# Performance work log

Measured on AMD Instinct MI355X. Metric: run time of the kernel, lower is better.

## Reference

```python
import jax, jax.numpy as jnp
import numpy as np

BETA = 0.25


def setup_inputs() -> dict:
    key = jax.random.key(0)
    k1, k2 = jax.random.split(key)
    z_e = jax.random.normal(k1, (16, 64, 64, 64), dtype=jnp.float32)  # (B, D, H, W)
    embedding = jax.random.normal(k2, (1024, 64), dtype=jnp.float32)  # (K, D)
    return {"z_e": z_e, "embedding": embedding}


def reference(z_e, embedding):
    B, D, H, W = z_e.shape
    # (B, D, H, W) -> (B, H, W, D) -> (N, D)
    flat = jnp.transpose(z_e, (0, 2, 3, 1)).reshape(-1, D)
    # squared L2 distances to codebook: (N, K)
    dist = (jnp.sum(flat * flat, axis=1, keepdims=True)
            + jnp.sum(embedding * embedding, axis=1)
            - 2.0 * flat @ embedding.T)
    indices = jnp.argmin(dist, axis=1)  # (N,)
    z_q_flat = embedding[indices]  # (N, D) gather
    z_q = jnp.transpose(z_q_flat.reshape(B, H, W, D), (0, 3, 1, 2))  # (B, D, H, W)
    codebook_loss = jnp.mean((jax.lax.stop_gradient(z_q) - z_e) ** 2)
    commit_loss = jnp.mean((z_q - jax.lax.stop_gradient(z_e)) ** 2)
    vq_loss = codebook_loss + BETA * commit_loss
    # straight-through estimator
    z_q_st = z_e + jax.lax.stop_gradient(z_q - z_e)
    return (z_q_st, vq_loss, indices.reshape(B, H, W))
```

## Files before the change

### kernel.cpp

```cpp
#include <hip/hip_runtime.h>
#include <math.h>

typedef short  short8 __attribute__((ext_vector_type(8)));
typedef float  f32x4  __attribute__((ext_vector_type(4)));

#define ZQ_ELEMS 4194304
#define KC       1024
#define EPS_HALF 0.005f
#define PXB      128


__device__ inline unsigned short bf16_rne(float f) {
    union { float fv; unsigned u; } a; a.fv = f;
    unsigned r = a.u + 0x7FFFu + ((a.u >> 16) & 1u);
    return (unsigned short)(r >> 16);
}
__device__ inline float bf16_to_f(unsigned short h) {
    union { unsigned u; float fv; } a; a.u = ((unsigned)h) << 16;
    return a.fv;
}
__device__ inline double dpack(float hi, unsigned lo) {
    return __hiloint2double(__float_as_int(hi), (int)lo);
}
__device__ inline float dhi(double d) { return __int_as_float(__double2hiint(d)); }
__device__ inline unsigned dlo(double d) { return (unsigned)__double2loint(d); }

__global__ __launch_bounds__(256) void vq_prep(const float* __restrict__ emb,
        unsigned short* __restrict__ epack, float* __restrict__ enorm,
        float* __restrict__ out) {
    const int k = blockIdx.x * 256 + threadIdx.x;
    if (k == 0) out[ZQ_ELEMS] = 0.f;
    const float4* e4 = (const float4*)(emb + k * 64);
    float s = 0.f;
#pragma unroll
    for (int j = 0; j < 16; ++j) {
        float4 v = e4[j];
        float vv[4] = {v.x, v.y, v.z, v.w};
        ushort4 hv, lv;
        unsigned short h[4], l[4];
#pragma unroll
        for (int t = 0; t < 4; ++t) {
            s = fmaf(vv[t], vv[t], s);
            h[t] = bf16_rne(vv[t]);
            l[t] = bf16_rne(vv[t] - bf16_to_f(h[t]));
        }
        hv.x = h[0]; hv.y = h[1]; hv.z = h[2]; hv.w = h[3];
        lv.x = l[0]; lv.y = l[1]; lv.z = l[2]; lv.w = l[3];
        *(ushort4*)(epack + k * 128 + j * 4)      = hv;
        *(ushort4*)(epack + k * 128 + 64 + j * 4) = lv;
    }
    enorm[k] = s;
}

__global__ __launch_bounds__(256, 2) void vq_scan(const float* __restrict__ z_e,
        const unsigned short* __restrict__ epack, const float* __restrict__ enorm,
        double* __restrict__ pbest, float* __restrict__ pb2) {
    const int tid  = threadIdx.x;
    const int lane = tid & 63;
    const int col  = lane & 15;
    const int g    = lane >> 4;
    const int wv   = __builtin_amdgcn_readfirstlane(tid >> 6);
    const int pxblock = blockIdx.x >> 2;
    const int grp     = blockIdx.x & 3;
    const int cbase   = grp * 256 + wv * 64;
    const int pblk    = pxblock * PXB;

    __shared__ __align__(16) unsigned short afrag[PXB * 128];
    __shared__ double mrgB[4][PXB];
    __shared__ float  mrgS[4][PXB];

    {
        const int lp   = tid & 127;
        const int half = tid >> 7;
        const int pg   = pblk + lp;
        const float* zb = z_e + (pg >> 12) * 262144 + (pg & 4095);
        const int sx = (lp & 7) << 3;
#pragma unroll
        for (int s8 = 0; s8 < 4; ++s8) {
            const int d0 = half * 32 + s8 * 8;
            short8 H, L;
#pragma unroll
            for (int j = 0; j < 8; ++j) {
                float v = zb[(d0 + j) * 4096];
                unsigned short h = bf16_rne(v);
                H[j] = (short)h;
                L[j] = (short)bf16_rne(v - bf16_to_f(h));
            }
            const int sw = d0 ^ sx;
            *(short8*)&afrag[lp * 128 + sw]      = H;
            *(short8*)&afrag[lp * 128 + 64 + sw] = L;
        }
    }

    short8 ah[4][2], al[4][2];
    f32x4 enf[4];
    int clo[4][4];
    const int K1 = 1023 - cbase - g * 4;
#pragma unroll
    for (int t = 0; t < 4; ++t) {
        const int code = cbase + t * 16 + col;
        const short8* ph = (const short8*)(epack + code * 128) + g;
        ah[t][0] = ph[0]; ah[t][1] = ph[4];
        al[t][0] = ph[8]; al[t][1] = ph[12];
        const float4 e4 = *(const float4*)(enorm + cbase + t * 16 + g * 4);
        enf[t][0] = -0.5f * e4.x; enf[t][1] = -0.5f * e4.y;
        enf[t][2] = -0.5f * e4.z; enf[t][3] = -0.5f * e4.w;
#pragma unroll
        for (int r = 0; r < 4; ++r) clo[t][r] = K1 - t * 16 - r;
    }
    __syncthreads();

    const f32x4 zero4 = {0.f, 0.f, 0.f, 0.f};
    const int g8 = g * 8;

#pragma unroll 2
    for (int it = 0; it < PXB / 16; ++it) {
        const int lpx = it * 16 + col;
        const int sxp = (lpx & 7) << 3;
        const unsigned short* ap = &afrag[lpx * 128];
        const short8 bh0 = *(const short8*)&ap[(g8        ) ^ sxp];
        const short8 bh1 = *(const short8*)&ap[(32 + g8   ) ^ sxp];
        const short8 bl0 = *(const short8*)&ap[64 + ((g8     ) ^ sxp)];
        const short8 bl1 = *(const short8*)&ap[64 + ((32 + g8) ^ sxp)];

        double B = dpack(-INFINITY, 0u);
        float  S = -INFINITY;
#pragma unroll
        for (int t = 0; t < 4; ++t) {
            f32x4 aA, aB;
            aA = __builtin_amdgcn_mfma_f32_16x16x32_bf16(ah[t][0], bh0, enf[t], 0, 0, 0);
            aB = __builtin_amdgcn_mfma_f32_16x16x32_bf16(ah[t][1], bh1, zero4, 0, 0, 0);
            aA = __builtin_amdgcn_mfma_f32_16x16x32_bf16(al[t][0], bh0, aA, 0, 0, 0);
            aB = __builtin_amdgcn_mfma_f32_16x16x32_bf16(al[t][1], bh1, aB, 0, 0, 0);
            aA = __builtin_amdgcn_mfma_f32_16x16x32_bf16(ah[t][0], bl0, aA, 0, 0, 0);
            aB = __builtin_amdgcn_mfma_f32_16x16x32_bf16(ah[t][1], bl1, aB, 0, 0, 0);
#pragma unroll
            for (int r = 0; r < 4; ++r) {
                const float v = aA[r] + aB[r];
                S = __builtin_amdgcn_fmed3f(dhi(B), S, v);
                B = fmax(B, dpack(v, (unsigned)clo[t][r]));
            }
        }
#pragma unroll
        for (int s = 16; s < 64; s <<= 1) {
            const double ob = __shfl_xor(B, s, 64);
            const float  o2 = __shfl_xor(S, s, 64);
            S = __builtin_amdgcn_fmed3f(dhi(B), dhi(ob), fmaxf(S, o2));
            B = fmax(B, ob);
        }
        if (g == 0) { mrgB[wv][lpx] = B; mrgS[wv][lpx] = S; }
    }

    __syncthreads();
    if (tid < PXB) {
        double B = mrgB[0][tid];
        float  S = mrgS[0][tid];
#pragma unroll
        for (int w = 1; w < 4; ++w) {
            const double ob = mrgB[w][tid];
            const float  o2 = mrgS[w][tid];
            S = __builtin_amdgcn_fmed3f(dhi(B), dhi(ob), fmaxf(S, o2));
            B = fmax(B, ob);
        }
        const int pxg = pblk + tid;
        pbest[grp * 65536 + pxg] = B;
        pb2[grp * 65536 + pxg]   = S;
    }
}

__global__ __launch_bounds__(256) void vq_final(const float* __restrict__ z_e,
        const float* __restrict__ emb, const double* __restrict__ pbest,
        const float* __restrict__ pb2, float* __restrict__ out) {
    __shared__ float zq[64][65];
    __shared__ int   sidx[64];
    __shared__ unsigned long long smask;
    __shared__ float sred[4];
    const int tid  = threadIdx.x;
    const int lane = tid & 63;
    const int w    = __builtin_amdgcn_readfirstlane(tid >> 6);
    const int pblk = blockIdx.x * 64;
    const int batch = pblk >> 12;
    const int hw0   = pblk & 4095;

    if (w == 0) {
        const int px = pblk + lane;
        double B = pbest[px];
        float  S = pb2[px];
#pragma unroll
        for (int gq = 1; gq < 4; ++gq) {
            const double ob = pbest[gq * 65536 + px];
            const float  o2 = pb2[gq * 65536 + px];
            S = __builtin_amdgcn_fmed3f(dhi(B), dhi(ob), fmaxf(S, o2));
            B = fmax(B, ob);
        }
        sidx[lane] = 1023 - (int)dlo(B);
        const unsigned long long m = __ballot(dhi(B) - S < EPS_HALF);
        if (lane == 0) smask = m;
    }
    __syncthreads();

    {
        unsigned long long m = smask;
        int item = 0;
        while (m) {
            const int i = __builtin_ctzll(m);
            m &= m - 1;
            if ((item & 3) == w) {
                const int pix = pblk + i;
                const float* zb = z_e + (pix >> 12) * 262144 + (pix & 4095);
                float f[64];
#pragma unroll
                for (int d = 0; d < 64; ++d) f[d] = zb[d * 4096];
                double best = INFINITY; int bk = KC;
                for (int j = 0; j < 16; ++j) {
                    const int k = j * 64 + lane;
                    const float* e = emb + k * 64;
                    double a0 = 0.0, a1 = 0.0;
#pragma unroll
                    for (int d = 0; d < 64; d += 2) {
                        double d0 = (double)f[d]     - (double)e[d];
                        double d1 = (double)f[d + 1] - (double)e[d + 1];
                        a0 = fma(d0, d0, a0);
                        a1 = fma(d1, d1, a1);
                    }
                    double acc = a0 + a1;
                    if (acc < best || (acc == best && k < bk)) { best = acc; bk = k; }
                }
                for (int off = 32; off; off >>= 1) {
                    double ov = __shfl_down(best, off, 64);
                    int    oi = __shfl_down(bk, off, 64);
                    if (ov < best || (ov == best && oi < bk)) { best = ov; bk = oi; }
                }
                if (lane == 0) sidx[i] = bk;
            }
            ++item;
        }
    }
    __syncthreads();

    if (tid < 64) out[ZQ_ELEMS + 1 + pblk + tid] = (float)sidx[tid];

#pragma unroll
    for (int i = 0; i < 16; ++i) {
        const int p = w * 16 + i;
        const int k = sidx[p];
        zq[p][lane] = emb[k * 64 + lane];
    }
    __syncthreads();

    const int p4 = (tid & 15) * 4;
    const float* zeb = z_e + batch * 262144 + hw0;
    float* ob = out + batch * 262144 + hw0;
    float ss = 0.f;
#pragma unroll
    for (int it = 0; it < 4; ++it) {
        const int d = (tid >> 4) + it * 16;
        float4 q;
        q.x = zq[p4 + 0][d]; q.y = zq[p4 + 1][d];
        q.z = zq[p4 + 2][d]; q.w = zq[p4 + 3][d];
        const float4 z = *(const float4*)(zeb + d * 4096 + p4);
        *(float4*)(ob + d * 4096 + p4) = q;
        const float d0 = q.x - z.x, d1 = q.y - z.y, d2 = q.z - z.z, d3 = q.w - z.w;
        ss += d0 * d0 + d1 * d1 + d2 * d2 + d3 * d3;
    }
    for (int off = 32; off; off >>= 1) ss += __shfl_down(ss, off, 64);
    if (lane == 0) sred[w] = ss;
    __syncthreads();
    if (tid == 0)
        atomicAdd(out + ZQ_ELEMS,
                  ((sred[0] + sred[1]) + (sred[2] + sred[3])) * (1.25f / (float)ZQ_ELEMS));
}

extern "C" void kernel_launch(void* const* d_in, const int* in_sizes, int n_in,
                              void* d_out, int out_size, void* d_ws, size_t ws_size,
                              hipStream_t stream) {
    const float* z_e = (const float*)d_in[0];
    const float* emb = (const float*)d_in[1];
    float* out = (float*)d_out;
    char* ws = (char*)d_ws;
    unsigned short* epack = (unsigned short*)ws;
    float*  enorm = (float*)(ws + 262144);
    double* pbest = (double*)(ws + 524288);
    float*  pb2   = (float*)(ws + 2621440);

    vq_prep<<<4, 256, 0, stream>>>(emb, epack, enorm, out);
    vq_scan<<<2048, 256, 0, stream>>>(z_e, epack, enorm, pbest, pb2);
    vq_final<<<1024, 256, 0, stream>>>(z_e, emb, pbest, pb2, out);
}
```

Baseline: 82.64 us.

## Fuse scan and finalize kernels into one per-64-pixel megakernel

Merges the codebook scan and the finalize pass into a single 512-thread kernel. Each block handles 64 pixels against the full codebook, with 8 waves each covering 128 codes across two register-loaded passes. The z_e tile stays in shared memory for the fp64 refinement and the loss, so z_e is read from global memory once instead of three times, and the pbest/pb2 workspace round trip is gone. In exchange, MFMA tiles per pass shrink from 8 to 4 pixel groups, so codebook fragments are reloaded per block. Blocks also carry larger shared memory and more serial phases, which may reduce overlap.

Result: slower. 89.42 us (+8.2%).

```diff
diff --git a/kernel.cpp b/kernel.cpp
--- a/kernel.cpp
+++ b/kernel.cpp
@@ -7,7 +7,6 @@
 #define ZQ_ELEMS 4194304
 #define KC       1024
 #define EPS_HALF 0.005f
-#define PXB      128
 
 
 __device__ inline unsigned short bf16_rne(float f) {
@@ -52,95 +51,107 @@
     enorm[k] = s;
 }
 
-__global__ __launch_bounds__(256, 2) void vq_scan(const float* __restrict__ z_e,
+__global__ __launch_bounds__(512) void vq_mega(const float* __restrict__ z_e,
         const unsigned short* __restrict__ epack, const float* __restrict__ enorm,
-        double* __restrict__ pbest, float* __restrict__ pb2) {
+        const float* __restrict__ emb, float* __restrict__ out) {
     const int tid  = threadIdx.x;
     const int lane = tid & 63;
     const int col  = lane & 15;
     const int g    = lane >> 4;
     const int wv   = __builtin_amdgcn_readfirstlane(tid >> 6);
-    const int pxblock = blockIdx.x >> 2;
-    const int grp     = blockIdx.x & 3;
-    const int cbase   = grp * 256 + wv * 64;
-    const int pblk    = pxblock * PXB;
-
-    __shared__ __align__(16) unsigned short afrag[PXB * 128];
-    __shared__ double mrgB[4][PXB];
-    __shared__ float  mrgS[4][PXB];
+    const int pblk = blockIdx.x * 64;
+
+    __shared__ float zfp[64][65];
+    __shared__ __align__(16) char ubuf[16640];
+    unsigned short* afrag = (unsigned short*)ubuf;
+    float (*zq)[65] = (float (*)[65])ubuf;
+    __shared__ double mrgB[8][64];
+    __shared__ float  mrgS[8][64];
+    __shared__ int    sidx[64];
+    __shared__ unsigned long long smask;
+    __shared__ float  sred[8];
 
     {
-        const int lp   = tid & 127;
-        const int half = tid >> 7;
-        const int pg   = pblk + lp;
+        const int pg = pblk + lane;
         const float* zb = z_e + (pg >> 12) * 262144 + (pg & 4095);
-        const int sx = (lp & 7) << 3;
-#pragma unroll
-        for (int s8 = 0; s8 < 4; ++s8) {
-            const int d0 = half * 32 + s8 * 8;
-            short8 H, L;
-#pragma unroll
-            for (int j = 0; j < 8; ++j) {
-                float v = zb[(d0 + j) * 4096];
-                unsigned short h = bf16_rne(v);
-                H[j] = (short)h;
-                L[j] = (short)bf16_rne(v - bf16_to_f(h));
-            }
-            const int sw = d0 ^ sx;
-            *(short8*)&afrag[lp * 128 + sw]      = H;
-            *(short8*)&afrag[lp * 128 + 64 + sw] = L;
-        }
-    }
-
-    short8 ah[4][2], al[4][2];
-    f32x4 enf[4];
-    int clo[4][4];
-    const int K1 = 1023 - cbase - g * 4;
-#pragma unroll
-    for (int t = 0; t < 4; ++t) {
-        const int code = cbase + t * 16 + col;
-        const short8* ph = (const short8*)(epack + code * 128) + g;
-        ah[t][0] = ph[0]; ah[t][1] = ph[4];
-        al[t][0] = ph[8]; al[t][1] = ph[12];
-        const float4 e4 = *(const float4*)(enorm + cbase + t * 16 + g * 4);
-        enf[t][0] = -0.5f * e4.x; enf[t][1] = -0.5f * e4.y;
-        enf[t][2] = -0.5f * e4.z; enf[t][3] = -0.5f * e4.w;
-#pragma unroll
-        for (int r = 0; r < 4; ++r) clo[t][r] = K1 - t * 16 - r;
-    }
-    __syncthreads();
+        const int d0 = wv * 8;
+        short8 H, L;
+#pragma unroll
+        for (int j = 0; j < 8; ++j) {
+            const float v = zb[(d0 + j) * 4096];
+            zfp[lane][d0 + j] = v;
+            const unsigned short h = bf16_rne(v);
+            H[j] = (short)h;
+            L[j] = (short)bf16_rne(v - bf16_to_f(h));
+        }
+        const int sw = d0 ^ ((lane & 7) << 3);
+        *(short8*)&afrag[lane * 128 + sw]      = H;
+        *(short8*)&afrag[lane * 128 + 64 + sw] = L;
+    }
+    __syncthreads();
+
+    double Brun[4];
+    float  Srun[4];
+#pragma unroll
+    for (int it = 0; it < 4; ++it) { Brun[it] = dpack(-INFINITY, 0u); Srun[it] = -INFINITY; }
 
     const f32x4 zero4 = {0.f, 0.f, 0.f, 0.f};
     const int g8 = g * 8;
 
-#pragma unroll 2
-    for (int it = 0; it < PXB / 16; ++it) {
-        const int lpx = it * 16 + col;
-        const int sxp = (lpx & 7) << 3;
-        const unsigned short* ap = &afrag[lpx * 128];
-        const short8 bh0 = *(const short8*)&ap[(g8        ) ^ sxp];
-        const short8 bh1 = *(const short8*)&ap[(32 + g8   ) ^ sxp];
-        const short8 bl0 = *(const short8*)&ap[64 + ((g8     ) ^ sxp)];
-        const short8 bl1 = *(const short8*)&ap[64 + ((32 + g8) ^ sxp)];
-
-        double B = dpack(-INFINITY, 0u);
-        float  S = -INFINITY;
+#pragma unroll 1
+    for (int grp = 0; grp < 2; ++grp) {
+        const int cbase = grp * 512 + wv * 64;
+        short8 ah[4][2], al[4][2];
+        f32x4 enf[4];
 #pragma unroll
         for (int t = 0; t < 4; ++t) {
-            f32x4 aA, aB;
-            aA = __builtin_amdgcn_mfma_f32_16x16x32_bf16(ah[t][0], bh0, enf[t], 0, 0, 0);
-            aB = __builtin_amdgcn_mfma_f32_16x16x32_bf16(ah[t][1], bh1, zero4, 0, 0, 0);
-            aA = __builtin_amdgcn_mfma_f32_16x16x32_bf16(al[t][0], bh0, aA, 0, 0, 0);
-            aB = __builtin_amdgcn_mfma_f32_16x16x32_bf16(al[t][1], bh1, aB, 0, 0, 0);
-            aA = __builtin_amdgcn_mfma_f32_16x16x32_bf16(ah[t][0], bl0, aA, 0, 0, 0);
-            aB = __builtin_amdgcn_mfma_f32_16x16x32_bf16(ah[t][1], bl1, aB, 0, 0, 0);
-#pragma unroll
-            for (int r = 0; r < 4; ++r) {
-                const float v = aA[r] + aB[r];
-                S = __builtin_amdgcn_fmed3f(dhi(B), S, v);
-                B = fmax(B, dpack(v, (unsigned)clo[t][r]));
+            const int code = cbase + t * 16 + col;
+            const short8* ph = (const short8*)(epack + code * 128) + g;
+            ah[t][0] = ph[0]; ah[t][1] = ph[4];
+            al[t][0] = ph[8]; al[t][1] = ph[12];
+            const float4 e4 = *(const float4*)(enorm + cbase + t * 16 + g * 4);
+            enf[t][0] = -0.5f * e4.x; enf[t][1] = -0.5f * e4.y;
+            enf[t][2] = -0.5f * e4.z; enf[t][3] = -0.5f * e4.w;
+        }
+        const int K1 = 1023 - cbase - g * 4;
+
+#pragma unroll
+        for (int it = 0; it < 4; ++it) {
+            const int lpx = it * 16 + col;
+            const int sxp = (lpx & 7) << 3;
+            const unsigned short* ap = &afrag[lpx * 128];
+            const short8 bh0 = *(const short8*)&ap[(g8     ) ^ sxp];
+            const short8 bh1 = *(const short8*)&ap[(32 + g8) ^ sxp];
+            const short8 bl0 = *(const short8*)&ap[64 + ((g8     ) ^ sxp)];
+            const short8 bl1 = *(const short8*)&ap[64 + ((32 + g8) ^ sxp)];
+
+            double B = Brun[it];
+            float  S = Srun[it];
+#pragma unroll
+            for (int t = 0; t < 4; ++t) {
+                f32x4 aA, aB;
+                aA = __builtin_amdgcn_mfma_f32_16x16x32_bf16(ah[t][0], bh0, enf[t], 0, 0, 0);
+                aB = __builtin_amdgcn_mfma_f32_16x16x32_bf16(ah[t][1], bh1, zero4, 0, 0, 0);
+                aA = __builtin_amdgcn_mfma_f32_16x16x32_bf16(al[t][0], bh0, aA, 0, 0, 0);
+                aB = __builtin_amdgcn_mfma_f32_16x16x32_bf16(al[t][1], bh1, aB, 0, 0, 0);
+                aA = __builtin_amdgcn_mfma_f32_16x16x32_bf16(ah[t][0], bl0, aA, 0, 0, 0);
+                aB = __builtin_amdgcn_mfma_f32_16x16x32_bf16(ah[t][1], bl1, aB, 0, 0, 0);
+#pragma unroll
+                for (int r = 0; r < 4; ++r) {
+                    const float v = aA[r] + aB[r];
+                    S = __builtin_amdgcn_fmed3f(dhi(B), S, v);
+                    B = fmax(B, dpack(v, (unsigned)(K1 - t * 16 - r)));
+                }
             }
-        }
+            Brun[it] = B;
+            Srun[it] = S;
+        }
+    }
+
+#pragma unroll
+    for (int it = 0; it < 4; ++it) {
+        double B = Brun[it];
+        float  S = Srun[it];
 #pragma unroll
         for (int s = 16; s < 64; s <<= 1) {
             const double ob = __shfl_xor(B, s, 64);
@@ -148,54 +159,23 @@
             S = __builtin_amdgcn_fmed3f(dhi(B), dhi(ob), fmaxf(S, o2));
             B = fmax(B, ob);
         }
-        if (g == 0) { mrgB[wv][lpx] = B; mrgS[wv][lpx] = S; }
-    }
-
-    __syncthreads();
-    if (tid < PXB) {
+        if (g == 0) { mrgB[wv][it * 16 + col] = B; mrgS[wv][it * 16 + col] = S; }
+    }
+    __syncthreads();
+
+    if (tid < 64) {
         double B = mrgB[0][tid];
         float  S = mrgS[0][tid];
 #pragma unroll
-        for (int w = 1; w < 4; ++w) {
+        for (int w = 1; w < 8; ++w) {
             const double ob = mrgB[w][tid];
             const float  o2 = mrgS[w][tid];
             S = __builtin_amdgcn_fmed3f(dhi(B), dhi(ob), fmaxf(S, o2));
             B = fmax(B, ob);
         }
-        const int pxg = pblk + tid;
-        pbest[grp * 65536 + pxg] = B;
-        pb2[grp * 65536 + pxg]   = S;
-    }
-}
-
-__global__ __launch_bounds__(256) void vq_final(const float* __restrict__ z_e,
-        const float* __restrict__ emb, const double* __restrict__ pbest,
-        const float* __restrict__ pb2, float* __restrict__ out) {
-    __shared__ float zq[64][65];
-    __shared__ int   sidx[64];
-    __shared__ unsigned long long smask;
-    __shared__ float sred[4];
-    const int tid  = threadIdx.x;
-    const int lane = tid & 63;
-    const int w    = __builtin_amdgcn_readfirstlane(tid >> 6);
-    const int pblk = blockIdx.x * 64;
-    const int batch = pblk >> 12;
-    const int hw0   = pblk & 4095;
-
-    if (w == 0) {
-        const int px = pblk + lane;
-        double B = pbest[px];
-        float  S = pb2[px];
-#pragma unroll
-        for (int gq = 1; gq < 4; ++gq) {
-            const double ob = pbest[gq * 65536 + px];
-            const float  o2 = pb2[gq * 65536 + px];
-            S = __builtin_amdgcn_fmed3f(dhi(B), dhi(ob), fmaxf(S, o2));
-            B = fmax(B, ob);
-        }
-        sidx[lane] = 1023 - (int)dlo(B);
+        sidx[tid] = 1023 - (int)dlo(B);
         const unsigned long long m = __ballot(dhi(B) - S < EPS_HALF);
-        if (lane == 0) smask = m;
+        if (tid == 0) smask = m;
     }
     __syncthreads();
 
@@ -205,12 +185,10 @@
         while (m) {
             const int i = __builtin_ctzll(m);
             m &= m - 1;
-            if ((item & 3) == w) {
-                const int pix = pblk + i;
-                const float* zb = z_e + (pix >> 12) * 262144 + (pix & 4095);
+            if ((item & 7) == wv) {
                 float f[64];
 #pragma unroll
-                for (int d = 0; d < 64; ++d) f[d] = zb[d * 4096];
+                for (int d = 0; d < 64; ++d) f[d] = zfp[i][d];
                 double best = INFINITY; int bk = KC;
                 for (int j = 0; j < 16; ++j) {
                     const int k = j * 64 + lane;
@@ -218,17 +196,17 @@
                     double a0 = 0.0, a1 = 0.0;
 #pragma unroll
                     for (int d = 0; d < 64; d += 2) {
-                        double d0 = (double)f[d]     - (double)e[d];
-                        double d1 = (double)f[d + 1] - (double)e[d + 1];
+                        const double d0 = (double)f[d]     - (double)e[d];
+                        const double d1 = (double)f[d + 1] - (double)e[d + 1];
                         a0 = fma(d0, d0, a0);
                         a1 = fma(d1, d1, a1);
                     }
-                    double acc = a0 + a1;
+                    const double acc = a0 + a1;
                     if (acc < best || (acc == best && k < bk)) { best = acc; bk = k; }
                 }
                 for (int off = 32; off; off >>= 1) {
-                    double ov = __shfl_down(best, off, 64);
-                    int    oi = __shfl_down(bk, off, 64);
+                    const double ov = __shfl_down(best, off, 64);
+                    const int    oi = __shfl_down(bk, off, 64);
                     if (ov < best || (ov == best && oi < bk)) { best = ov; bk = oi; }
                 }
                 if (lane == 0) sidx[i] = bk;
@@ -241,34 +219,40 @@
     if (tid < 64) out[ZQ_ELEMS + 1 + pblk + tid] = (float)sidx[tid];
 
 #pragma unroll
-    for (int i = 0; i < 16; ++i) {
-        const int p = w * 16 + i;
+    for (int i = 0; i < 8; ++i) {
+        const int p = wv * 8 + i;
         const int k = sidx[p];
         zq[p][lane] = emb[k * 64 + lane];
     }
     __syncthreads();
 
     const int p4 = (tid & 15) * 4;
-    const float* zeb = z_e + batch * 262144 + hw0;
+    const int dd = tid >> 4;
+    const int batch = pblk >> 12;
+    const int hw0   = pblk & 4095;
     float* ob = out + batch * 262144 + hw0;
     float ss = 0.f;
 #pragma unroll
-    for (int it = 0; it < 4; ++it) {
-        const int d = (tid >> 4) + it * 16;
+    for (int h = 0; h < 2; ++h) {
+        const int d = dd + h * 32;
         float4 q;
         q.x = zq[p4 + 0][d]; q.y = zq[p4 + 1][d];
         q.z = zq[p4 + 2][d]; q.w = zq[p4 + 3][d];
-        const float4 z = *(const float4*)(zeb + d * 4096 + p4);
+        const float z0 = zfp[p4 + 0][d], z1 = zfp[p4 + 1][d];
+        const float z2 = zfp[p4 + 2][d], z3 = zfp[p4 + 3][d];
         *(float4*)(ob + d * 4096 + p4) = q;
-        const float d0 = q.x - z.x, d1 = q.y - z.y, d2 = q.z - z.z, d3 = q.w - z.w;
-        ss += d0 * d0 + d1 * d1 + d2 * d2 + d3 * d3;
+        const float e0 = q.x - z0, e1 = q.y - z1, e2 = q.z - z2, e3 = q.w - z3;
+        ss += e0 * e0 + e1 * e1 + e2 * e2 + e3 * e3;
     }
     for (int off = 32; off; off >>= 1) ss += __shfl_down(ss, off, 64);
-    if (lane == 0) sred[w] = ss;
-    __syncthreads();
-    if (tid == 0)
-        atomicAdd(out + ZQ_ELEMS,
-                  ((sred[0] + sred[1]) + (sred[2] + sred[3])) * (1.25f / (float)ZQ_ELEMS));
+    if (lane == 0) sred[wv] = ss;
+    __syncthreads();
+    if (tid == 0) {
+        float tot = 0.f;
+#pragma unroll
+        for (int w = 0; w < 8; ++w) tot += sred[w];
+        atomicAdd(out + ZQ_ELEMS, tot * (1.25f / (float)ZQ_ELEMS));
+    }
 }
 
 extern "C" void kernel_launch(void* const* d_in, const int* in_sizes, int n_in,
@@ -279,11 +263,8 @@
     float* out = (float*)d_out;
     char* ws = (char*)d_ws;
     unsigned short* epack = (unsigned short*)ws;
-    float*  enorm = (float*)(ws + 262144);
-    double* pbest = (double*)(ws + 524288);
-    float*  pb2   = (float*)(ws + 2621440);
+    float* enorm = (float*)(ws + 262144);
 
     vq_prep<<<4, 256, 0, stream>>>(emb, epack, enorm, out);
-    vq_scan<<<2048, 256, 0, stream>>>(z_e, epack, enorm, pbest, pb2);
-    vq_final<<<1024, 256, 0, stream>>>(z_e, emb, pbest, pb2, out);
-}
+    vq_mega<<<1024, 512, 0, stream>>>(z_e, epack, enorm, emb, out);
+}
```

## Defer near-tie fp64 rechecks to a separate compacted fix-up kernel

Applied to the files above, without the earlier changes.

Pixels whose best and second-best scores lie within the tie margin are no longer rechecked inline in vq_final, where a single risky pixel stalls a whole block. Instead they are appended to a global list through an atomic counter, and a new vq_fix kernel re-scans the codebook in fp64 with a shared-memory embedding tile. When the chosen code changes, it patches the index, the z_q column and the loss using the distance delta. This removes load imbalance in vq_final but adds a fourth kernel launch, atomics, and an in-place correction of the loss sum.

After: 84.15 us. About the same (+1.8%).

```diff
diff --git a/kernel.cpp b/kernel.cpp
--- a/kernel.cpp
+++ b/kernel.cpp
@@ -27,9 +27,9 @@
 
 __global__ __launch_bounds__(256) void vq_prep(const float* __restrict__ emb,
         unsigned short* __restrict__ epack, float* __restrict__ enorm,
-        float* __restrict__ out) {
+        int* __restrict__ risky_cnt, float* __restrict__ out) {
     const int k = blockIdx.x * 256 + threadIdx.x;
-    if (k == 0) out[ZQ_ELEMS] = 0.f;
+    if (k == 0) { *risky_cnt = 0; out[ZQ_ELEMS] = 0.f; }
     const float4* e4 = (const float4*)(emb + k * 64);
     float s = 0.f;
 #pragma unroll
@@ -170,10 +170,10 @@
 
 __global__ __launch_bounds__(256) void vq_final(const float* __restrict__ z_e,
         const float* __restrict__ emb, const double* __restrict__ pbest,
-        const float* __restrict__ pb2, float* __restrict__ out) {
+        const float* __restrict__ pb2, float* __restrict__ out,
+        int* __restrict__ risky_cnt, int* __restrict__ risky) {
     __shared__ float zq[64][65];
     __shared__ int   sidx[64];
-    __shared__ unsigned long long smask;
     __shared__ float sred[4];
     const int tid  = threadIdx.x;
     const int lane = tid & 63;
@@ -193,52 +193,17 @@
             S = __builtin_amdgcn_fmed3f(dhi(B), dhi(ob), fmaxf(S, o2));
             B = fmax(B, ob);
         }
-        sidx[lane] = 1023 - (int)dlo(B);
-        const unsigned long long m = __ballot(dhi(B) - S < EPS_HALF);
-        if (lane == 0) smask = m;
-    }
-    __syncthreads();
-
-    {
-        unsigned long long m = smask;
-        int item = 0;
-        while (m) {
-            const int i = __builtin_ctzll(m);
-            m &= m - 1;
-            if ((item & 3) == w) {
-                const int pix = pblk + i;
-                const float* zb = z_e + (pix >> 12) * 262144 + (pix & 4095);
-                float f[64];
-#pragma unroll
-                for (int d = 0; d < 64; ++d) f[d] = zb[d * 4096];
-                double best = INFINITY; int bk = KC;
-                for (int j = 0; j < 16; ++j) {
-                    const int k = j * 64 + lane;
-                    const float* e = emb + k * 64;
-                    double a0 = 0.0, a1 = 0.0;
-#pragma unroll
-                    for (int d = 0; d < 64; d += 2) {
-                        double d0 = (double)f[d]     - (double)e[d];
-                        double d1 = (double)f[d + 1] - (double)e[d + 1];
-                        a0 = fma(d0, d0, a0);
-                        a1 = fma(d1, d1, a1);
-                    }
-                    double acc = a0 + a1;
-                    if (acc < best || (acc == best && k < bk)) { best = acc; bk = k; }
-                }
-                for (int off = 32; off; off >>= 1) {
-                    double ov = __shfl_down(best, off, 64);
-                    int    oi = __shfl_down(bk, off, 64);
-                    if (ov < best || (ov == best && oi < bk)) { best = ov; bk = oi; }
-                }
-                if (lane == 0) sidx[i] = bk;
-            }
-            ++item;
-        }
-    }
-    __syncthreads();
-
-    if (tid < 64) out[ZQ_ELEMS + 1 + pblk + tid] = (float)sidx[tid];
+        const int idx = 1023 - (int)dlo(B);
+        sidx[lane] = idx;
+        out[ZQ_ELEMS + 1 + px] = (float)idx;
+        const bool risk = (dhi(B) - S < EPS_HALF);
+        const unsigned long long m = __ballot(risk);
+        int base = 0;
+        if (lane == 0 && m) base = atomicAdd(risky_cnt, __popcll(m));
+        base = __shfl(base, 0, 64);
+        if (risk) risky[base + __popcll(m & ((1ull << lane) - 1ull))] = px;
+    }
+    __syncthreads();
 
 #pragma unroll
     for (int i = 0; i < 16; ++i) {
@@ -260,8 +225,8 @@
         q.z = zq[p4 + 2][d]; q.w = zq[p4 + 3][d];
         const float4 z = *(const float4*)(zeb + d * 4096 + p4);
         *(float4*)(ob + d * 4096 + p4) = q;
-        const float d0 = q.x - z.x, d1 = q.y - z.y, d2 = q.z - z.z, d3 = q.w - z.w;
-        ss += d0 * d0 + d1 * d1 + d2 * d2 + d3 * d3;
+        const float e0 = q.x - z.x, e1 = q.y - z.y, e2 = q.z - z.z, e3 = q.w - z.w;
+        ss += e0 * e0 + e1 * e1 + e2 * e2 + e3 * e3;
     }
     for (int off = 32; off; off >>= 1) ss += __shfl_down(ss, off, 64);
     if (lane == 0) sred[w] = ss;
@@ -269,6 +234,74 @@
     if (tid == 0)
         atomicAdd(out + ZQ_ELEMS,
                   ((sred[0] + sred[1]) + (sred[2] + sred[3])) * (1.25f / (float)ZQ_ELEMS));
+}
+
+__global__ __launch_bounds__(256) void vq_fix(const float* __restrict__ z_e,
+        const float* __restrict__ emb, float* __restrict__ out,
+        const int* __restrict__ cnt, const int* __restrict__ list) {
+    const int n = *cnt;
+    if ((int)blockIdx.x * 4 >= n) return;
+    __shared__ float etile[64][65];
+    const int tid  = threadIdx.x;
+    const int lane = tid & 63;
+    const int wv   = __builtin_amdgcn_readfirstlane(tid >> 6);
+
+    for (int base = blockIdx.x * 4; base < n; base += gridDim.x * 4) {
+        const int item = base + wv;
+        const bool active = item < n;
+        int pix = 0, oldk = 0;
+        float f[64];
+        if (active) {
+            pix = list[item];
+            const float* zb = z_e + (pix >> 12) * 262144 + (pix & 4095);
+#pragma unroll
+            for (int d = 0; d < 64; ++d) f[d] = zb[d * 4096];
+            oldk = (int)out[ZQ_ELEMS + 1 + pix];
+        }
+        double best = INFINITY; int bk = KC;
+        double dold = 0.0;
+        for (int j = 0; j < 16; ++j) {
+            __syncthreads();
+#pragma unroll
+            for (int i = 0; i < 16; ++i) {
+                const int idx = i * 256 + tid;
+                etile[idx >> 6][idx & 63] = emb[j * 4096 + idx];
+            }
+            __syncthreads();
+            if (active) {
+                const int k = j * 64 + lane;
+                double a0 = 0.0, a1 = 0.0;
+#pragma unroll
+                for (int d = 0; d < 64; d += 2) {
+                    const double d0 = (double)f[d]     - (double)etile[lane][d];
+                    const double d1 = (double)f[d + 1] - (double)etile[lane][d + 1];
+                    a0 = fma(d0, d0, a0);
+                    a1 = fma(d1, d1, a1);
+                }
+                const double acc = a0 + a1;
+                if (acc < best || (acc == best && k < bk)) { best = acc; bk = k; }
+                if (k == oldk) dold = acc;
+            }
+        }
+        if (active) {
+            for (int off = 32; off; off >>= 1) {
+                const double ov = __shfl_down(best, off, 64);
+                const int    oi = __shfl_down(bk, off, 64);
+                if (ov < best || (ov == best && oi < bk)) { best = ov; bk = oi; }
+            }
+            for (int off = 32; off; off >>= 1) dold += __shfl_down(dold, off, 64);
+            bk   = __shfl(bk, 0, 64);
+            best = __shfl(best, 0, 64);
+            dold = __shfl(dold, 0, 64);
+            if (bk != oldk) {
+                if (lane == 0) out[ZQ_ELEMS + 1 + pix] = (float)bk;
+                out[(pix >> 12) * 262144 + (pix & 4095) + lane * 4096] = emb[bk * 64 + lane];
+                if (lane == 0)
+                    atomicAdd(out + ZQ_ELEMS,
+                              (float)((best - dold) * (1.25 / (double)ZQ_ELEMS)));
+            }
+        }
+    }
 }
 
 extern "C" void kernel_launch(void* const* d_in, const int* in_sizes, int n_in,
@@ -279,11 +312,14 @@
     float* out = (float*)d_out;
     char* ws = (char*)d_ws;
     unsigned short* epack = (unsigned short*)ws;
-    float*  enorm = (float*)(ws + 262144);
-    double* pbest = (double*)(ws + 524288);
-    float*  pb2   = (float*)(ws + 2621440);
-
-    vq_prep<<<4, 256, 0, stream>>>(emb, epack, enorm, out);
+    float*  enorm     = (float*)(ws + 262144);
+    int*    risky_cnt = (int*)(ws + 266240);
+    int*    risky     = (int*)(ws + 270336);
+    double* pbest     = (double*)(ws + 524288);
+    float*  pb2       = (float*)(ws + 2621440);
+
+    vq_prep<<<4, 256, 0, stream>>>(emb, epack, enorm, risky_cnt, out);
     vq_scan<<<2048, 256, 0, stream>>>(z_e, epack, enorm, pbest, pb2);
-    vq_final<<<1024, 256, 0, stream>>>(z_e, emb, pbest, pb2, out);
-}
+    vq_final<<<1024, 256, 0, stream>>>(z_e, emb, pbest, pb2, out, risky_cnt, risky);
+    vq_fix<<<512, 256, 0, stream>>>(z_e, emb, out, risky_cnt, risky);
+}
```
